# Kernel tuning notes

Hardware: AMD Instinct MI355X
Metric: run time of the kernel (lower is better)

The kernel has to match this reference:

```python
import jax, jax.numpy as jnp
import numpy as np

N_USERS = 200000
N_ITEMS = 100000
N_EDGES = 1000000
D = 64
NUM_LAYERS = 3
BATCH = 8192


def setup_inputs() -> dict:
    key = jax.random.key(0)
    ks = jax.random.split(key, 8)
    return {
        "user_feat": jax.random.normal(ks[0], (N_USERS, D), dtype=jnp.float32) * 0.1,
        "item_feat": jax.random.normal(ks[1], (N_ITEMS, D), dtype=jnp.float32) * 0.1,
        "edge_u": jax.random.randint(ks[2], (N_EDGES,), 0, N_USERS, dtype=jnp.int32),
        "edge_i": jax.random.randint(ks[3], (N_EDGES,), 0, N_ITEMS, dtype=jnp.int32),
        "norm": jax.random.uniform(ks[4], (N_EDGES,), dtype=jnp.float32),
        "users": jax.random.randint(ks[5], (BATCH,), 0, N_USERS, dtype=jnp.int32),
        "pos_items": jax.random.randint(ks[6], (BATCH,), 0, N_ITEMS, dtype=jnp.int32),
        "neg_items": jax.random.randint(ks[7], (BATCH,), 0, N_ITEMS, dtype=jnp.int32),
    }


def reference(user_feat, item_feat, edge_u, edge_i, norm, users, pos_items, neg_items):
    # LightGCN propagation: each layer does edge-weighted gather-scatter
    # (u_mul_e 'h','norm' -> sum) in both directions of the bipartite graph.
    u_h, i_h = user_feat, item_feat
    u_acc, i_acc = u_h, i_h
    w = norm[:, None]  # [E, 1]
    for _ in range(NUM_LAYERS):
        # user -> item messages
        new_i = jax.ops.segment_sum(u_h[edge_u] * w, edge_i, num_segments=N_ITEMS)
        # item -> user messages
        new_u = jax.ops.segment_sum(i_h[edge_i] * w, edge_u, num_segments=N_USERS)
        u_h, i_h = new_u, new_i
        u_acc = u_acc + u_h
        i_acc = i_acc + i_h
    scale = 1.0 / (NUM_LAYERS + 1)
    u_acc = u_acc * scale
    i_acc = i_acc * scale
    return (u_acc[users], i_acc[pos_items], i_acc[neg_items])
```

## Files before the change

### kernel.cpp

```cpp
#include <hip/hip_runtime.h>


#define N_USERS 200000
#define N_ITEMS 100000
#define N_EDGES 1000000
#define DIM 64
#define BATCH 8192
#define NTOT (N_USERS + N_ITEMS)
#define NOUT (3 * BATCH)
#define NPART 293
#define PLOCAL 1024
#define CAP 11264

#define HA 489
#define NUNITS (NTOT * DIM / 8)
#define CB ((NUNITS + 1023) / 1024)
#define OB (NOUT * 8 / 256)
#define AB8 (NTOT / 32)
#define FB ((NOUT + 255) / 256)

__device__ __forceinline__ unsigned f2bf(float f) {
    unsigned u = __float_as_uint(f);
    return (u + 0x7fffu + ((u >> 16) & 1u)) >> 16;
}
__device__ __forceinline__ uint2 pack4(float4 v) {
    uint2 o;
    o.x = f2bf(v.x) | (f2bf(v.y) << 16);
    o.y = f2bf(v.z) | (f2bf(v.w) << 16);
    return o;
}
__device__ __forceinline__ void fma4(float4& a, uint2 v, float w) {
    a.x += __uint_as_float(v.x << 16) * w;
    a.y += __uint_as_float(v.x & 0xffff0000u) * w;
    a.z += __uint_as_float(v.y << 16) * w;
    a.w += __uint_as_float(v.y & 0xffff0000u) * w;
}
__device__ __forceinline__ int out_bucket(int orow, const int* users,
                                          const int* pos, const int* neg) {
    int seg = orow >> 13;
    int b = orow & (BATCH - 1);
    if (seg == 0) return users[b];
    if (seg == 1) return N_USERS + pos[b];
    return N_USERS + neg[b];
}

__global__ void partition_conv_kernel(const int* __restrict__ eu,
                                      const int* __restrict__ ei,
                                      const float* __restrict__ w,
                                      int* __restrict__ gcur,
                                      uint2* __restrict__ partBuf,
                                      const float4* __restrict__ uf4,
                                      const float4* __restrict__ if4,
                                      unsigned short* __restrict__ F0,
                                      const float* __restrict__ u_feat,
                                      const float* __restrict__ i_feat,
                                      const int* __restrict__ users,
                                      const int* __restrict__ pos,
                                      const int* __restrict__ neg,
                                      float* __restrict__ out)
{
    int bid = blockIdx.x, t = threadIdx.x;
    if (bid < HA) {
        __shared__ int lh[NPART];
        __shared__ int lcur[NPART];
        for (int k = t; k < NPART; k += 256) lh[k] = 0;
        __syncthreads();
        int e0 = (bid * 256 + t) * 8;
        bool act = e0 < N_EDGES;
        int4 u0, u1, i0, i1;
        if (act) {
            u0 = *reinterpret_cast<const int4*>(eu + e0);
            u1 = *reinterpret_cast<const int4*>(eu + e0 + 4);
            i0 = *reinterpret_cast<const int4*>(ei + e0);
            i1 = *reinterpret_cast<const int4*>(ei + e0 + 4);
            atomicAdd(&lh[u0.x >> 10], 1);
            atomicAdd(&lh[u0.y >> 10], 1);
            atomicAdd(&lh[u0.z >> 10], 1);
            atomicAdd(&lh[u0.w >> 10], 1);
            atomicAdd(&lh[u1.x >> 10], 1);
            atomicAdd(&lh[u1.y >> 10], 1);
            atomicAdd(&lh[u1.z >> 10], 1);
            atomicAdd(&lh[u1.w >> 10], 1);
            atomicAdd(&lh[(N_USERS + i0.x) >> 10], 1);
            atomicAdd(&lh[(N_USERS + i0.y) >> 10], 1);
            atomicAdd(&lh[(N_USERS + i0.z) >> 10], 1);
            atomicAdd(&lh[(N_USERS + i0.w) >> 10], 1);
            atomicAdd(&lh[(N_USERS + i1.x) >> 10], 1);
            atomicAdd(&lh[(N_USERS + i1.y) >> 10], 1);
            atomicAdd(&lh[(N_USERS + i1.z) >> 10], 1);
            atomicAdd(&lh[(N_USERS + i1.w) >> 10], 1);
        }
        __syncthreads();
        for (int k = t; k < NPART; k += 256) {
            int v = lh[k];
            lcur[k] = v ? atomicAdd(&gcur[k], v) : 0;
        }
        __syncthreads();
        if (act) {
            float4 wa = *reinterpret_cast<const float4*>(w + e0);
            float4 wb = *reinterpret_cast<const float4*>(w + e0 + 4);
            int us[8] = {u0.x, u0.y, u0.z, u0.w, u1.x, u1.y, u1.z, u1.w};
            int is[8] = {i0.x, i0.y, i0.z, i0.w, i1.x, i1.y, i1.z, i1.w};
            float ws[8] = {wa.x, wa.y, wa.z, wa.w, wb.x, wb.y, wb.z, wb.w};
            #pragma unroll
            for (int j = 0; j < 8; ++j) {
                int bu = us[j];
                int bi = N_USERS + is[j];
                unsigned wbits = __float_as_uint(ws[j]);
                int pu = bu >> 10, pi = bi >> 10;
                int su = atomicAdd(&lcur[pu], 1);
                partBuf[(size_t)pu * CAP + su] =
                    make_uint2((unsigned)(bu & 1023) | ((unsigned)bi << 10), wbits);
                int si = atomicAdd(&lcur[pi], 1);
                partBuf[(size_t)pi * CAP + si] =
                    make_uint2((unsigned)(bi & 1023) | ((unsigned)bu << 10), wbits);
            }
        }
    } else if (bid < HA + CB) {
        const int NU4 = N_USERS * DIM / 4;
        int jb = (bid - HA) * 1024 + t;
        float4 a[4], b[4];
        #pragma unroll
        for (int c = 0; c < 4; ++c) {
            int j = jb + c * 256;
            if (j < NUNITS) {
                int f4 = j * 2;
                if (f4 < NU4) { a[c] = uf4[f4];       b[c] = uf4[f4 + 1]; }
                else          { a[c] = if4[f4 - NU4]; b[c] = if4[f4 - NU4 + 1]; }
            }
        }
        #pragma unroll
        for (int c = 0; c < 4; ++c) {
            int j = jb + c * 256;
            if (j < NUNITS) {
                uint2 pa = pack4(a[c]), pb = pack4(b[c]);
                *reinterpret_cast<uint4*>(F0 + (size_t)j * 8) =
                    make_uint4(pa.x, pa.y, pb.x, pb.y);
            }
        }
    } else {
        int idx = (bid - HA - CB) * 256 + t;
        int row = idx >> 3;
        if (row >= NOUT) return;
        int d8 = (idx & 7) << 3;
        int seg = row >> 13;
        int b = row & (BATCH - 1);
        const float* src;
        if (seg == 0)      src = u_feat + (size_t)users[b] * DIM;
        else if (seg == 1) src = i_feat + (size_t)pos[b]   * DIM;
        else               src = i_feat + (size_t)neg[b]   * DIM;
        float4 v0 = *reinterpret_cast<const float4*>(src + d8);
        float4 v1 = *reinterpret_cast<const float4*>(src + d8 + 4);
        v0.x *= 0.25f; v0.y *= 0.25f; v0.z *= 0.25f; v0.w *= 0.25f;
        v1.x *= 0.25f; v1.y *= 0.25f; v1.z *= 0.25f; v1.w *= 0.25f;
        float* op = out + (size_t)row * DIM + d8;
        *reinterpret_cast<float4*>(op) = v0;
        *reinterpret_cast<float4*>(op + 4) = v1;
    }
}

__global__ void __launch_bounds__(1024)
build_csr_kernel(const int* __restrict__ gcur,
                 const uint2* __restrict__ partBuf,
                 int2* __restrict__ rp2,
                 int2* __restrict__ entries)
{
    __shared__ int h[PLOCAL];
    __shared__ int s[PLOCAL];
    __shared__ int cur[PLOCAL];
    int p = blockIdx.x, t = threadIdx.x;
    int base = p * CAP;
    int end = base + gcur[p];
    h[t] = 0;
    __syncthreads();
    for (int r = base + t; r < end; r += 1024)
        atomicAdd(&h[partBuf[r].x & 1023], 1);
    __syncthreads();
    s[t] = h[t];
    __syncthreads();
    for (int off = 1; off < 1024; off <<= 1) {
        int x = (t >= off) ? s[t - off] : 0;
        __syncthreads();
        s[t] += x;
        __syncthreads();
    }
    int c0 = base + s[t] - h[t];
    cur[t] = c0;
    int gb = p * PLOCAL + t;
    if (gb < NTOT) rp2[gb] = make_int2(c0, h[t]);
    __syncthreads();
    for (int r = base + t; r < end; r += 1024) {
        uint2 rec = partBuf[r];
        int slot = atomicAdd(&cur[rec.x & 1023], 1);
        entries[slot] = make_int2((int)(rec.x >> 10), (int)rec.y);
    }
}

__device__ __forceinline__ void agg_row8(int2 rc, int l8, int gb,
                                         const int2* __restrict__ entries,
                                         const unsigned short* __restrict__ src,
                                         float4& sL, float4& sH)
{
    int beg = rc.x, cnt = rc.y;
    float4 a0L = {0,0,0,0}, a0H = {0,0,0,0}, a1L = {0,0,0,0}, a1H = {0,0,0,0};
    for (int base = 0; base < cnt; base += 8) {
        int2 e = make_int2(0, 0);
        if (base + l8 < cnt) e = entries[beg + base + l8];
        int   c[8];
        float wv[8];
        #pragma unroll
        for (int k = 0; k < 8; ++k) {
            c[k]  = __shfl(e.x, gb + k);
            wv[k] = __int_as_float(__shfl(e.y, gb + k));
        }
        uint4 v[8];
        #pragma unroll
        for (int k = 0; k < 8; ++k)
            v[k] = *reinterpret_cast<const uint4*>(
                src + (size_t)c[k] * DIM + l8 * 8);
        #pragma unroll
        for (int k = 0; k < 8; ++k) {
            if (k & 1) {
                fma4(a1L, make_uint2(v[k].x, v[k].y), wv[k]);
                fma4(a1H, make_uint2(v[k].z, v[k].w), wv[k]);
            } else {
                fma4(a0L, make_uint2(v[k].x, v[k].y), wv[k]);
                fma4(a0H, make_uint2(v[k].z, v[k].w), wv[k]);
            }
        }
    }
    sL.x = a0L.x + a1L.x; sL.y = a0L.y + a1L.y;
    sL.z = a0L.z + a1L.z; sL.w = a0L.w + a1L.w;
    sH.x = a0H.x + a1H.x; sH.y = a0H.y + a1H.y;
    sH.z = a0H.z + a1H.z; sH.w = a0H.w + a1H.w;
}

__global__ void agg1_flag_kernel(const int2* __restrict__ rp2,
                                 const int2* __restrict__ entries,
                                 const unsigned short* __restrict__ F0,
                                 unsigned short* __restrict__ H1,
                                 const int* __restrict__ users,
                                 const int* __restrict__ pos,
                                 const int* __restrict__ neg,
                                 int* __restrict__ flags)
{
    int bid = blockIdx.x;
    if (bid < AB8) {
        int gid = bid * 256 + threadIdx.x;
        int lane = gid & 63;
        int l8 = lane & 7;
        int gb = lane & 56;
        int row = gid >> 3;
        if (row >= NTOT) return;
        float4 sL, sH;
        agg_row8(rp2[row], l8, gb, entries, F0, sL, sH);
        uint2 pL = pack4(sL), pH = pack4(sH);
        *reinterpret_cast<uint4*>(H1 + (size_t)row * DIM + l8 * 8) =
            make_uint4(pL.x, pL.y, pH.x, pH.y);
    } else {
        int t = (bid - AB8) * 256 + threadIdx.x;
        if (t >= NOUT) return;
        int bucket = out_bucket(t, users, pos, neg);
        flags[bucket] = 1;
        int2 rc = rp2[bucket];
        for (int k = rc.x; k < rc.x + rc.y; ++k)
            flags[entries[k].x] = 1;
    }
}

__global__ void compact_kernel(const int* __restrict__ flags,
                               int* __restrict__ list,
                               int* __restrict__ count)
{
    int t = blockIdx.x * blockDim.x + threadIdx.x;
    int idx = t * 4;
    if (idx >= NTOT) return;
    int4 f = *reinterpret_cast<const int4*>(flags + idx);
    int loc[4]; int k = 0;
    if (f.x) loc[k++] = idx;
    if (f.y) loc[k++] = idx + 1;
    if (f.z) loc[k++] = idx + 2;
    if (f.w) loc[k++] = idx + 3;
    if (k) {
        int base = atomicAdd(count, k);
        for (int m = 0; m < k; ++m) list[base + m] = loc[m];
    }
}

__global__ void agg2_add1_kernel(const int2* __restrict__ rp2,
                                 const int2* __restrict__ entries,
                                 const unsigned short* __restrict__ H1,
                                 unsigned short* __restrict__ H2,
                                 const int* __restrict__ list,
                                 const int* __restrict__ count,
                                 const int* __restrict__ users,
                                 const int* __restrict__ pos,
                                 const int* __restrict__ neg,
                                 float* __restrict__ out)
{
    int bid = blockIdx.x;
    if (bid < AB8) {
        int gid = bid * 256 + threadIdx.x;
        int lane = gid & 63;
        int l8 = lane & 7;
        int gb = lane & 56;
        int idx = gid >> 3;
        int n = *count;
        if (idx >= n) return;
        int row = list[idx];
        float4 sL, sH;
        agg_row8(rp2[row], l8, gb, entries, H1, sL, sH);
        uint2 pL = pack4(sL), pH = pack4(sH);
        *reinterpret_cast<uint4*>(H2 + (size_t)row * DIM + l8 * 8) =
            make_uint4(pL.x, pL.y, pH.x, pH.y);
    } else {
        int idx = (bid - AB8) * 256 + threadIdx.x;
        int row = idx >> 3;
        if (row >= NOUT) return;
        int d8 = (idx & 7) << 3;
        int bucket = out_bucket(row, users, pos, neg);
        uint4 v = *reinterpret_cast<const uint4*>(H1 + (size_t)bucket * DIM + d8);
        float* op = out + (size_t)row * DIM + d8;
        float4 o0 = *reinterpret_cast<const float4*>(op);
        float4 o1 = *reinterpret_cast<const float4*>(op + 4);
        o0.x += 0.25f * __uint_as_float(v.x << 16);
        o0.y += 0.25f * __uint_as_float(v.x & 0xffff0000u);
        o0.z += 0.25f * __uint_as_float(v.y << 16);
        o0.w += 0.25f * __uint_as_float(v.y & 0xffff0000u);
        o1.x += 0.25f * __uint_as_float(v.z << 16);
        o1.y += 0.25f * __uint_as_float(v.z & 0xffff0000u);
        o1.z += 0.25f * __uint_as_float(v.w << 16);
        o1.w += 0.25f * __uint_as_float(v.w & 0xffff0000u);
        *reinterpret_cast<float4*>(op) = o0;
        *reinterpret_cast<float4*>(op + 4) = o1;
    }
}

__global__ void aggout_add2_kernel(const int2* __restrict__ rp2,
                                   const int2* __restrict__ entries,
                                   const unsigned short* __restrict__ H2,
                                   const int* __restrict__ users,
                                   const int* __restrict__ pos,
                                   const int* __restrict__ neg,
                                   float* __restrict__ out)
{
    int gid = blockIdx.x * 256 + threadIdx.x;
    int lane = gid & 63;
    int l8 = lane & 7;
    int gb = lane & 56;
    int orow = gid >> 3;
    if (orow >= NOUT) return;
    int bucket = out_bucket(orow, users, pos, neg);
    float4 sL, sH;
    agg_row8(rp2[bucket], l8, gb, entries, H2, sL, sH);
    uint4 v = *reinterpret_cast<const uint4*>(H2 + (size_t)bucket * DIM + l8 * 8);
    sL.x += __uint_as_float(v.x << 16);
    sL.y += __uint_as_float(v.x & 0xffff0000u);
    sL.z += __uint_as_float(v.y << 16);
    sL.w += __uint_as_float(v.y & 0xffff0000u);
    sH.x += __uint_as_float(v.z << 16);
    sH.y += __uint_as_float(v.z & 0xffff0000u);
    sH.z += __uint_as_float(v.w << 16);
    sH.w += __uint_as_float(v.w & 0xffff0000u);
    float* op = out + (size_t)orow * DIM + l8 * 8;
    float4 o0 = *reinterpret_cast<const float4*>(op);
    float4 o1 = *reinterpret_cast<const float4*>(op + 4);
    o0.x += 0.25f * sL.x; o0.y += 0.25f * sL.y;
    o0.z += 0.25f * sL.z; o0.w += 0.25f * sL.w;
    o1.x += 0.25f * sH.x; o1.y += 0.25f * sH.y;
    o1.z += 0.25f * sH.z; o1.w += 0.25f * sH.w;
    *reinterpret_cast<float4*>(op) = o0;
    *reinterpret_cast<float4*>(op + 4) = o1;
}

extern "C" void kernel_launch(void* const* d_in, const int* in_sizes, int n_in,
                              void* d_out, int out_size, void* d_ws, size_t ws_size,
                              hipStream_t stream)
{
    const float* user_feat = (const float*)d_in[0];
    const float* item_feat = (const float*)d_in[1];
    const int*   eu        = (const int*)d_in[2];
    const int*   ei        = (const int*)d_in[3];
    const float* norm      = (const float*)d_in[4];
    const int*   users     = (const int*)d_in[5];
    const int*   pos       = (const int*)d_in[6];
    const int*   neg       = (const int*)d_in[7];
    float* out = (float*)d_out;

    auto align256 = [](size_t x) { return (x + 255) & ~(size_t)255; };
    const size_t hBytes = (size_t)NTOT * DIM * sizeof(unsigned short);
    const size_t pBytes = (size_t)NPART * CAP * 8;

    char* p = (char*)d_ws;
    unsigned short* F0 = (unsigned short*)p; p += align256(hBytes);
    unsigned short* H1 = (unsigned short*)p; p += align256(hBytes);
    unsigned short* H2 = (unsigned short*)p; p += align256(hBytes);
    int* gcur = (int*)p; p += align256((size_t)(512 + NTOT + 16) * 4);
    int* flags = gcur + 512;
    int* count = flags + NTOT;
    int2* rp2      = (int2*)p;  p += align256((size_t)NTOT * 8);
    uint2* partBuf = (uint2*)p; p += align256(pBytes);
    int*  list     = (int*)p;   p += align256((size_t)NTOT * 4);
    int2* entries  = (int2*)p;  p += align256(pBytes);

    hipMemsetAsync(gcur, 0, (size_t)(512 + NTOT + 16) * 4, stream);

    partition_conv_kernel<<<HA + CB + OB, 256, 0, stream>>>(
        eu, ei, norm, gcur, partBuf,
        (const float4*)user_feat, (const float4*)item_feat, F0,
        user_feat, item_feat, users, pos, neg, out);

    build_csr_kernel<<<NPART, 1024, 0, stream>>>(gcur, partBuf, rp2, entries);

    agg1_flag_kernel<<<AB8 + FB, 256, 0, stream>>>(
        rp2, entries, F0, H1, users, pos, neg, flags);

    compact_kernel<<<(NTOT / 4 + 255) / 256, 256, 0, stream>>>(flags, list, count);

    agg2_add1_kernel<<<AB8 + OB, 256, 0, stream>>>(
        rp2, entries, H1, H2, list, count, users, pos, neg, out);

    aggout_add2_kernel<<<NOUT / 32, 256, 0, stream>>>(
        rp2, entries, H2, users, pos, neg, out);
}
```

Measured before the change: 271.8 us.

## Compute 2-hop frontier flags during edge scatter and fuse compact into CSR build

Adds a prep kernel that marks output buckets in a byte mask. The edge scatter then sets neighbor flags directly whenever an endpoint is an output row, which replaces the later pass that walked each output row's CSR adjacency. The bf16 conversion and flag compaction move into the CSR-build launch as extra blocks, so one launch disappears and they share the grid with the per-partition build. The cost is an extra byte-mask lookup and possible global flag writes per edge in the scatter, plus one additional small kernel launch.

After: 267.2 us. Within noise of the previous version (-1.7%).

```diff
diff --git a/kernel.cpp b/kernel.cpp
--- a/kernel.cpp
+++ b/kernel.cpp
@@ -14,10 +14,12 @@
 
 #define HA 489
 #define NUNITS (NTOT * DIM / 8)
-#define CB ((NUNITS + 1023) / 1024)
 #define OB (NOUT * 8 / 256)
 #define AB8 (NTOT / 32)
-#define FB ((NOUT + 255) / 256)
+#define PRB (NOUT / 1024)
+#define PHB (NOUT * 8 / 1024)
+#define CVB ((NUNITS + 4095) / 4096)
+#define CPB ((NTOT / 4 + 1023) / 1024)
 
 __device__ __forceinline__ unsigned f2bf(float f) {
     unsigned u = __float_as_uint(f);
@@ -44,104 +46,25 @@
     return N_USERS + neg[b];
 }
 
-__global__ void partition_conv_kernel(const int* __restrict__ eu,
-                                      const int* __restrict__ ei,
-                                      const float* __restrict__ w,
-                                      int* __restrict__ gcur,
-                                      uint2* __restrict__ partBuf,
-                                      const float4* __restrict__ uf4,
-                                      const float4* __restrict__ if4,
-                                      unsigned short* __restrict__ F0,
-                                      const float* __restrict__ u_feat,
-                                      const float* __restrict__ i_feat,
-                                      const int* __restrict__ users,
-                                      const int* __restrict__ pos,
-                                      const int* __restrict__ neg,
-                                      float* __restrict__ out)
+__global__ void __launch_bounds__(1024)
+prep_kernel(const int* __restrict__ users,
+            const int* __restrict__ pos,
+            const int* __restrict__ neg,
+            const float* __restrict__ u_feat,
+            const float* __restrict__ i_feat,
+            unsigned char* __restrict__ isOut,
+            int* __restrict__ flags,
+            float* __restrict__ out)
 {
     int bid = blockIdx.x, t = threadIdx.x;
-    if (bid < HA) {
-        __shared__ int lh[NPART];
-        __shared__ int lcur[NPART];
-        for (int k = t; k < NPART; k += 256) lh[k] = 0;
-        __syncthreads();
-        int e0 = (bid * 256 + t) * 8;
-        bool act = e0 < N_EDGES;
-        int4 u0, u1, i0, i1;
-        if (act) {
-            u0 = *reinterpret_cast<const int4*>(eu + e0);
-            u1 = *reinterpret_cast<const int4*>(eu + e0 + 4);
-            i0 = *reinterpret_cast<const int4*>(ei + e0);
-            i1 = *reinterpret_cast<const int4*>(ei + e0 + 4);
-            atomicAdd(&lh[u0.x >> 10], 1);
-            atomicAdd(&lh[u0.y >> 10], 1);
-            atomicAdd(&lh[u0.z >> 10], 1);
-            atomicAdd(&lh[u0.w >> 10], 1);
-            atomicAdd(&lh[u1.x >> 10], 1);
-            atomicAdd(&lh[u1.y >> 10], 1);
-            atomicAdd(&lh[u1.z >> 10], 1);
-            atomicAdd(&lh[u1.w >> 10], 1);
-            atomicAdd(&lh[(N_USERS + i0.x) >> 10], 1);
-            atomicAdd(&lh[(N_USERS + i0.y) >> 10], 1);
-            atomicAdd(&lh[(N_USERS + i0.z) >> 10], 1);
-            atomicAdd(&lh[(N_USERS + i0.w) >> 10], 1);
-            atomicAdd(&lh[(N_USERS + i1.x) >> 10], 1);
-            atomicAdd(&lh[(N_USERS + i1.y) >> 10], 1);
-            atomicAdd(&lh[(N_USERS + i1.z) >> 10], 1);
-            atomicAdd(&lh[(N_USERS + i1.w) >> 10], 1);
-        }
-        __syncthreads();
-        for (int k = t; k < NPART; k += 256) {
-            int v = lh[k];
-            lcur[k] = v ? atomicAdd(&gcur[k], v) : 0;
-        }
-        __syncthreads();
-        if (act) {
-            float4 wa = *reinterpret_cast<const float4*>(w + e0);
-            float4 wb = *reinterpret_cast<const float4*>(w + e0 + 4);
-            int us[8] = {u0.x, u0.y, u0.z, u0.w, u1.x, u1.y, u1.z, u1.w};
-            int is[8] = {i0.x, i0.y, i0.z, i0.w, i1.x, i1.y, i1.z, i1.w};
-            float ws[8] = {wa.x, wa.y, wa.z, wa.w, wb.x, wb.y, wb.z, wb.w};
-            #pragma unroll
-            for (int j = 0; j < 8; ++j) {
-                int bu = us[j];
-                int bi = N_USERS + is[j];
-                unsigned wbits = __float_as_uint(ws[j]);
-                int pu = bu >> 10, pi = bi >> 10;
-                int su = atomicAdd(&lcur[pu], 1);
-                partBuf[(size_t)pu * CAP + su] =
-                    make_uint2((unsigned)(bu & 1023) | ((unsigned)bi << 10), wbits);
-                int si = atomicAdd(&lcur[pi], 1);
-                partBuf[(size_t)pi * CAP + si] =
-                    make_uint2((unsigned)(bi & 1023) | ((unsigned)bu << 10), wbits);
-            }
-        }
-    } else if (bid < HA + CB) {
-        const int NU4 = N_USERS * DIM / 4;
-        int jb = (bid - HA) * 1024 + t;
-        float4 a[4], b[4];
-        #pragma unroll
-        for (int c = 0; c < 4; ++c) {
-            int j = jb + c * 256;
-            if (j < NUNITS) {
-                int f4 = j * 2;
-                if (f4 < NU4) { a[c] = uf4[f4];       b[c] = uf4[f4 + 1]; }
-                else          { a[c] = if4[f4 - NU4]; b[c] = if4[f4 - NU4 + 1]; }
-            }
-        }
-        #pragma unroll
-        for (int c = 0; c < 4; ++c) {
-            int j = jb + c * 256;
-            if (j < NUNITS) {
-                uint2 pa = pack4(a[c]), pb = pack4(b[c]);
-                *reinterpret_cast<uint4*>(F0 + (size_t)j * 8) =
-                    make_uint4(pa.x, pa.y, pb.x, pb.y);
-            }
-        }
+    if (bid < PRB) {
+        int orow = bid * 1024 + t;
+        int bucket = out_bucket(orow, users, pos, neg);
+        isOut[bucket] = 1;
+        flags[bucket] = 1;
     } else {
-        int idx = (bid - HA - CB) * 256 + t;
+        int idx = (bid - PRB) * 1024 + t;
         int row = idx >> 3;
-        if (row >= NOUT) return;
         int d8 = (idx & 7) << 3;
         int seg = row >> 13;
         int b = row & (BATCH - 1);
@@ -159,40 +82,152 @@
     }
 }
 
+__global__ void scatter_kernel(const int* __restrict__ eu,
+                               const int* __restrict__ ei,
+                               const float* __restrict__ w,
+                               int* __restrict__ gcur,
+                               uint2* __restrict__ partBuf,
+                               const unsigned char* __restrict__ isOut,
+                               int* __restrict__ flags)
+{
+    __shared__ int lh[NPART];
+    __shared__ int lcur[NPART];
+    int bid = blockIdx.x, t = threadIdx.x;
+    for (int k = t; k < NPART; k += 256) lh[k] = 0;
+    __syncthreads();
+    int e0 = (bid * 256 + t) * 8;
+    bool act = e0 < N_EDGES;
+    int4 u0, u1, i0, i1;
+    if (act) {
+        u0 = *reinterpret_cast<const int4*>(eu + e0);
+        u1 = *reinterpret_cast<const int4*>(eu + e0 + 4);
+        i0 = *reinterpret_cast<const int4*>(ei + e0);
+        i1 = *reinterpret_cast<const int4*>(ei + e0 + 4);
+        atomicAdd(&lh[u0.x >> 10], 1);
+        atomicAdd(&lh[u0.y >> 10], 1);
+        atomicAdd(&lh[u0.z >> 10], 1);
+        atomicAdd(&lh[u0.w >> 10], 1);
+        atomicAdd(&lh[u1.x >> 10], 1);
+        atomicAdd(&lh[u1.y >> 10], 1);
+        atomicAdd(&lh[u1.z >> 10], 1);
+        atomicAdd(&lh[u1.w >> 10], 1);
+        atomicAdd(&lh[(N_USERS + i0.x) >> 10], 1);
+        atomicAdd(&lh[(N_USERS + i0.y) >> 10], 1);
+        atomicAdd(&lh[(N_USERS + i0.z) >> 10], 1);
+        atomicAdd(&lh[(N_USERS + i0.w) >> 10], 1);
+        atomicAdd(&lh[(N_USERS + i1.x) >> 10], 1);
+        atomicAdd(&lh[(N_USERS + i1.y) >> 10], 1);
+        atomicAdd(&lh[(N_USERS + i1.z) >> 10], 1);
+        atomicAdd(&lh[(N_USERS + i1.w) >> 10], 1);
+    }
+    __syncthreads();
+    for (int k = t; k < NPART; k += 256) {
+        int v = lh[k];
+        lcur[k] = v ? atomicAdd(&gcur[k], v) : 0;
+    }
+    __syncthreads();
+    if (act) {
+        float4 wa = *reinterpret_cast<const float4*>(w + e0);
+        float4 wb = *reinterpret_cast<const float4*>(w + e0 + 4);
+        int us[8] = {u0.x, u0.y, u0.z, u0.w, u1.x, u1.y, u1.z, u1.w};
+        int is[8] = {i0.x, i0.y, i0.z, i0.w, i1.x, i1.y, i1.z, i1.w};
+        float ws[8] = {wa.x, wa.y, wa.z, wa.w, wb.x, wb.y, wb.z, wb.w};
+        #pragma unroll
+        for (int j = 0; j < 8; ++j) {
+            int bu = us[j];
+            int bi = N_USERS + is[j];
+            unsigned wbits = __float_as_uint(ws[j]);
+            int pu = bu >> 10, pi = bi >> 10;
+            int su = atomicAdd(&lcur[pu], 1);
+            partBuf[(size_t)pu * CAP + su] =
+                make_uint2((unsigned)(bu & 1023) | ((unsigned)bi << 10), wbits);
+            int si = atomicAdd(&lcur[pi], 1);
+            partBuf[(size_t)pi * CAP + si] =
+                make_uint2((unsigned)(bi & 1023) | ((unsigned)bu << 10), wbits);
+            if (isOut[bu]) flags[bi] = 1;
+            if (isOut[bi]) flags[bu] = 1;
+        }
+    }
+}
+
 __global__ void __launch_bounds__(1024)
-build_csr_kernel(const int* __restrict__ gcur,
-                 const uint2* __restrict__ partBuf,
-                 int2* __restrict__ rp2,
-                 int2* __restrict__ entries)
+mid_kernel(const int* __restrict__ gcur,
+           const uint2* __restrict__ partBuf,
+           int2* __restrict__ rp2,
+           int2* __restrict__ entries,
+           const float4* __restrict__ uf4,
+           const float4* __restrict__ if4,
+           unsigned short* __restrict__ F0,
+           const int* __restrict__ flags,
+           int* __restrict__ list,
+           int* __restrict__ count)
 {
     __shared__ int h[PLOCAL];
     __shared__ int s[PLOCAL];
     __shared__ int cur[PLOCAL];
-    int p = blockIdx.x, t = threadIdx.x;
-    int base = p * CAP;
-    int end = base + gcur[p];
-    h[t] = 0;
-    __syncthreads();
-    for (int r = base + t; r < end; r += 1024)
-        atomicAdd(&h[partBuf[r].x & 1023], 1);
-    __syncthreads();
-    s[t] = h[t];
-    __syncthreads();
-    for (int off = 1; off < 1024; off <<= 1) {
-        int x = (t >= off) ? s[t - off] : 0;
+    int bid = blockIdx.x, t = threadIdx.x;
+    if (bid < NPART) {
+        int p = bid;
+        int base = p * CAP;
+        int end = base + gcur[p];
+        h[t] = 0;
         __syncthreads();
-        s[t] += x;
+        for (int r = base + t; r < end; r += 1024)
+            atomicAdd(&h[partBuf[r].x & 1023], 1);
         __syncthreads();
-    }
-    int c0 = base + s[t] - h[t];
-    cur[t] = c0;
-    int gb = p * PLOCAL + t;
-    if (gb < NTOT) rp2[gb] = make_int2(c0, h[t]);
-    __syncthreads();
-    for (int r = base + t; r < end; r += 1024) {
-        uint2 rec = partBuf[r];
-        int slot = atomicAdd(&cur[rec.x & 1023], 1);
-        entries[slot] = make_int2((int)(rec.x >> 10), (int)rec.y);
+        s[t] = h[t];
+        __syncthreads();
+        for (int off = 1; off < 1024; off <<= 1) {
+            int x = (t >= off) ? s[t - off] : 0;
+            __syncthreads();
+            s[t] += x;
+            __syncthreads();
+        }
+        int c0 = base + s[t] - h[t];
+        cur[t] = c0;
+        int gb = p * PLOCAL + t;
+        if (gb < NTOT) rp2[gb] = make_int2(c0, h[t]);
+        __syncthreads();
+        for (int r = base + t; r < end; r += 1024) {
+            uint2 rec = partBuf[r];
+            int slot = atomicAdd(&cur[rec.x & 1023], 1);
+            entries[slot] = make_int2((int)(rec.x >> 10), (int)rec.y);
+        }
+    } else if (bid < NPART + CVB) {
+        const int NU4 = N_USERS * DIM / 4;
+        int jb = (bid - NPART) * 4096 + t;
+        float4 a[4], b[4];
+        #pragma unroll
+        for (int c = 0; c < 4; ++c) {
+            int j = jb + c * 1024;
+            if (j < NUNITS) {
+                int f4 = j * 2;
+                if (f4 < NU4) { a[c] = uf4[f4];       b[c] = uf4[f4 + 1]; }
+                else          { a[c] = if4[f4 - NU4]; b[c] = if4[f4 - NU4 + 1]; }
+            }
+        }
+        #pragma unroll
+        for (int c = 0; c < 4; ++c) {
+            int j = jb + c * 1024;
+            if (j < NUNITS) {
+                uint2 pa = pack4(a[c]), pb = pack4(b[c]);
+                *reinterpret_cast<uint4*>(F0 + (size_t)j * 8) =
+                    make_uint4(pa.x, pa.y, pb.x, pb.y);
+            }
+        }
+    } else {
+        int idx = ((bid - NPART - CVB) * 1024 + t) * 4;
+        if (idx >= NTOT) return;
+        int4 f = *reinterpret_cast<const int4*>(flags + idx);
+        int loc[4]; int k = 0;
+        if (f.x) loc[k++] = idx;
+        if (f.y) loc[k++] = idx + 1;
+        if (f.z) loc[k++] = idx + 2;
+        if (f.w) loc[k++] = idx + 3;
+        if (k) {
+            int base = atomicAdd(count, k);
+            for (int m = 0; m < k; ++m) list[base + m] = loc[m];
+        }
     }
 }
 
@@ -235,56 +270,22 @@
     sH.z = a0H.z + a1H.z; sH.w = a0H.w + a1H.w;
 }
 
-__global__ void agg1_flag_kernel(const int2* __restrict__ rp2,
-                                 const int2* __restrict__ entries,
-                                 const unsigned short* __restrict__ F0,
-                                 unsigned short* __restrict__ H1,
-                                 const int* __restrict__ users,
-                                 const int* __restrict__ pos,
-                                 const int* __restrict__ neg,
-                                 int* __restrict__ flags)
-{
-    int bid = blockIdx.x;
-    if (bid < AB8) {
-        int gid = bid * 256 + threadIdx.x;
-        int lane = gid & 63;
-        int l8 = lane & 7;
-        int gb = lane & 56;
-        int row = gid >> 3;
-        if (row >= NTOT) return;
-        float4 sL, sH;
-        agg_row8(rp2[row], l8, gb, entries, F0, sL, sH);
-        uint2 pL = pack4(sL), pH = pack4(sH);
-        *reinterpret_cast<uint4*>(H1 + (size_t)row * DIM + l8 * 8) =
-            make_uint4(pL.x, pL.y, pH.x, pH.y);
-    } else {
-        int t = (bid - AB8) * 256 + threadIdx.x;
-        if (t >= NOUT) return;
-        int bucket = out_bucket(t, users, pos, neg);
-        flags[bucket] = 1;
-        int2 rc = rp2[bucket];
-        for (int k = rc.x; k < rc.x + rc.y; ++k)
-            flags[entries[k].x] = 1;
-    }
-}
-
-__global__ void compact_kernel(const int* __restrict__ flags,
-                               int* __restrict__ list,
-                               int* __restrict__ count)
-{
-    int t = blockIdx.x * blockDim.x + threadIdx.x;
-    int idx = t * 4;
-    if (idx >= NTOT) return;
-    int4 f = *reinterpret_cast<const int4*>(flags + idx);
-    int loc[4]; int k = 0;
-    if (f.x) loc[k++] = idx;
-    if (f.y) loc[k++] = idx + 1;
-    if (f.z) loc[k++] = idx + 2;
-    if (f.w) loc[k++] = idx + 3;
-    if (k) {
-        int base = atomicAdd(count, k);
-        for (int m = 0; m < k; ++m) list[base + m] = loc[m];
-    }
+__global__ void agg1_kernel(const int2* __restrict__ rp2,
+                            const int2* __restrict__ entries,
+                            const unsigned short* __restrict__ F0,
+                            unsigned short* __restrict__ H1)
+{
+    int gid = blockIdx.x * 256 + threadIdx.x;
+    int lane = gid & 63;
+    int l8 = lane & 7;
+    int gb = lane & 56;
+    int row = gid >> 3;
+    if (row >= NTOT) return;
+    float4 sL, sH;
+    agg_row8(rp2[row], l8, gb, entries, F0, sL, sH);
+    uint2 pL = pack4(sL), pH = pack4(sH);
+    *reinterpret_cast<uint4*>(H1 + (size_t)row * DIM + l8 * 8) =
+        make_uint4(pL.x, pL.y, pH.x, pH.y);
 }
 
 __global__ void agg2_add1_kernel(const int2* __restrict__ rp2,
@@ -395,27 +396,31 @@
     unsigned short* F0 = (unsigned short*)p; p += align256(hBytes);
     unsigned short* H1 = (unsigned short*)p; p += align256(hBytes);
     unsigned short* H2 = (unsigned short*)p; p += align256(hBytes);
-    int* gcur = (int*)p; p += align256((size_t)(512 + NTOT + 16) * 4);
+    const size_t zBytes = (size_t)(512 + NTOT + 16) * 4 + NTOT;
+    int* gcur = (int*)p;
     int* flags = gcur + 512;
     int* count = flags + NTOT;
+    unsigned char* isOut = (unsigned char*)(count + 16);
+    p += align256(zBytes);
     int2* rp2      = (int2*)p;  p += align256((size_t)NTOT * 8);
     uint2* partBuf = (uint2*)p; p += align256(pBytes);
     int*  list     = (int*)p;   p += align256((size_t)NTOT * 4);
     int2* entries  = (int2*)p;  p += align256(pBytes);
 
-    hipMemsetAsync(gcur, 0, (size_t)(512 + NTOT + 16) * 4, stream);
-
-    partition_conv_kernel<<<HA + CB + OB, 256, 0, stream>>>(
-        eu, ei, norm, gcur, partBuf,
+    hipMemsetAsync(gcur, 0, zBytes, stream);
+
+    prep_kernel<<<PRB + PHB, 1024, 0, stream>>>(
+        users, pos, neg, user_feat, item_feat, isOut, flags, out);
+
+    scatter_kernel<<<HA, 256, 0, stream>>>(
+        eu, ei, norm, gcur, partBuf, isOut, flags);
+
+    mid_kernel<<<NPART + CVB + CPB, 1024, 0, stream>>>(
+        gcur, partBuf, rp2, entries,
         (const float4*)user_feat, (const float4*)item_feat, F0,
-        user_feat, item_feat, users, pos, neg, out);
-
-    build_csr_kernel<<<NPART, 1024, 0, stream>>>(gcur, partBuf, rp2, entries);
-
-    agg1_flag_kernel<<<AB8 + FB, 256, 0, stream>>>(
-        rp2, entries, F0, H1, users, pos, neg, flags);
-
-    compact_kernel<<<(NTOT / 4 + 255) / 256, 256, 0, stream>>>(flags, list, count);
+        flags, list, count);
+
+    agg1_kernel<<<AB8, 256, 0, stream>>>(rp2, entries, F0, H1);
 
     agg2_add1_kernel<<<AB8 + OB, 256, 0, stream>>>(
         rp2, entries, H1, H2, list, count, users, pos, neg, out);
```
